# Optimization experiments

Hardware: AMD Instinct MI355X
Metric: run time of the kernel (lower is better)

## Reference

```python
import jax, jax.numpy as jnp
import numpy as np

B, T = 16, 100
MCL = 100      # MAX_CODE_LEN
D_IN = 200     # input_dim (= ques_encoding)
D_BERT = 768
KC = 50        # KC_one_hot_dim
KCD = 100      # kc_embed_dim
HID = 128
SCALE_BERT = 100
TW = 0.5       # QPALA_config.total_attention_weight
BTW = 0.5      # BLAA_config.total_attention_weight


def setup_inputs():
    key = jax.random.key(0)
    ks = jax.random.split(key, 20)
    f32 = jnp.float32
    # composite input feature vector: [ques_enc | code2vec idx | bert | time | score | kc one-hot]
    rnn_first = (jax.random.uniform(ks[0], (B, T, D_IN)) < 0.1).astype(f32)
    c2v = jax.random.randint(ks[1], (B, T, 3 * MCL), 0, 10000).astype(f32)
    bert = jax.random.normal(ks[2], (B, T, D_BERT), f32)
    time_f = jax.random.uniform(ks[3], (B, T, 10), f32)
    score_f = jax.random.uniform(ks[4], (B, T, 2), f32)
    kc = (jax.random.uniform(ks[5], (B, T, KC)) < 0.15).astype(f32)
    x = jnp.concatenate([rnn_first, c2v, bert, time_f, score_f, kc], axis=2)  # [B,T,1330]
    s = 0.05
    p = lambda k, shp: jax.random.normal(k, shp, f32) * s
    return dict(
        x=x,
        node_emb=p(ks[6], (10002, 100)),
        path_emb=p(ks[7], (20002, 100)),
        Wb=p(ks[8], (SCALE_BERT, D_BERT)), bb=jnp.zeros((SCALE_BERT,), f32),
        Wna=p(ks[9], (500, 500)), bna=jnp.zeros((500,), f32),
        Wia=p(ks[10], (KCD, 500)), bia=jnp.zeros((KCD,), f32),
        Wattn=p(ks[11], (1, 500)), battn=jnp.zeros((1,), f32),
        kc_emb=p(ks[12], (KC, KCD)),
        Wt=p(ks[13], (1, SCALE_BERT + KC + KCD)), bt=jnp.zeros((1,), f32),
        Wih=p(ks[14], (4 * HID, 950)), Whh=p(ks[15], (4 * HID, HID)),
        bih=jnp.zeros((4 * HID,), f32), bhh=jnp.zeros((4 * HID,), f32),
        Wfc=p(ks[16], (100, HID + KC + D_IN)), bfc=jnp.zeros((100,), f32),
    )


def _lstm(xseq, Wih, Whh, bih, bhh):
    # PyTorch LSTM, gate order i,f,g,o; batch_first
    bsz = xseq.shape[0]
    pre = jnp.einsum('btd,gd->btg', xseq, Wih) + bih + bhh  # [B,T,4H]

    def step(carry, g_in):
        h, c = carry
        g = g_in + h @ Whh.T
        i, f, gg, o = jnp.split(g, 4, axis=-1)
        c = jax.nn.sigmoid(f) * c + jax.nn.sigmoid(i) * jnp.tanh(gg)
        h = jax.nn.sigmoid(o) * jnp.tanh(c)
        return (h, c), h

    init = (jnp.zeros((bsz, HID), xseq.dtype), jnp.zeros((bsz, HID), xseq.dtype))
    _, hs = jax.lax.scan(step, init, jnp.swapaxes(pre, 0, 1))
    return jnp.swapaxes(hs, 0, 1)


def _forward(x, node_emb, path_emb, Wb, bb, Wna, bna, Wia, bia, Wattn, battn,
             kc_emb, Wt, bt, Wih, Whh, bih, bhh, Wfc, bfc):
    b, t = x.shape[0], x.shape[1]
    rnn_first = x[:, :, :D_IN]
    bert = x[:, :, 500:500 + D_BERT]
    kc_part = x[:, :, 1280:1280 + KC]
    c2v = x[:, :, D_IN:D_IN + 3 * MCL].reshape(b, t, MCL, 3).astype(jnp.int32)
    # gather embeddings + broadcast encoding -> full_embed [B,T,MCL,500]
    full = jnp.concatenate([
        node_emb[c2v[..., 0]], node_emb[c2v[..., 2]], path_emb[c2v[..., 1]],
        jnp.broadcast_to(rnn_first[:, :, None, :], (b, t, MCL, D_IN))], axis=3)
    bert_vec = bert @ Wb.T + bb  # [B,T,100]
    # non-interactive attention pooling (NB: original softmaxes over dim=1 = time)
    cw = jnp.tanh(full @ Wna.T + bna) @ Wattn.T + battn  # [B,T,MCL,1]
    aw = jax.nn.softmax(cw, axis=1)
    na = jnp.sum(full * aw, axis=2)  # [B,T,500]
    kcn = jnp.sum(kc_part, axis=2, keepdims=True)
    kcn = jnp.where(kcn == 0, 1.0, kcn)
    # interactive (KC) cross attention
    trans = full @ Wia.T + bia  # [B,T,MCL,KCD]
    Q = kc_part[..., None] * kc_emb[None, None]  # [B,T,KC,KCD]
    attn = jax.nn.softmax(jnp.einsum('btkd,btmd->btkm', Q, trans), axis=-1)
    Hm = jnp.einsum('btkm,btmd->btkd', attn, trans) * kc_part[..., None]
    ia = jnp.sum(Hm, axis=2) / kcn  # [B,T,KCD]
    rnn_input = jnp.concatenate([kc_part, rnn_first, ia, na, bert_vec], axis=2)  # [B,T,950]
    lstm_out = _lstm(rnn_input, Wih, Whh, bih, bhh)  # [B,T,HID]
    # per-time-step causal attention over lstm_out (vectorized form of the python loop)
    w = (jnp.concatenate([bert_vec, kc_part, ia], axis=2) @ Wt.T + bt)[..., 0]  # [B,T]
    mask = jnp.tril(jnp.ones((t, t), bool))
    logits = jnp.where(mask[None], w[:, None, :], -1e30)
    cattn = jax.nn.softmax(logits, axis=-1)  # [B,T,T]
    cur = jnp.einsum('bij,bjh->bih', cattn, lstm_out)
    attended = lstm_out * (1.0 - TW)
    attended = attended.at[:, 0].set(lstm_out[:, 0])
    idx = jnp.arange(t)
    addm = ((idx >= 1) & (idx <= t - 2)).astype(x.dtype)[None, :, None]
    attended = attended + cur * BTW * addm
    out = jax.nn.sigmoid(
        jnp.concatenate([rnn_first, kc_part, attended], axis=2) @ Wfc.T + bfc)
    return out  # [B,T,100]


def reference(x, node_emb, path_emb, Wb, bb, Wna, bna, Wia, bia, Wattn, battn,
              kc_emb, Wt, bt, Wih, Whh, bih, bhh, Wfc, bfc):
    return _forward(x, node_emb, path_emb, Wb, bb, Wna, bna, Wia, bia, Wattn, battn,
                    kc_emb, Wt, bt, Wih, Whh, bih, bhh, Wfc, bfc)
```

## Files before the change

### kernel.cpp

```cpp
#include <hip/hip_runtime.h>
#include <math.h>

typedef unsigned short ushort_t;
typedef unsigned char uchar_t;
typedef __attribute__((ext_vector_type(8))) short bf16x8;
typedef __attribute__((ext_vector_type(4))) float f32x4;

constexpr int CB = 16, CT = 100, CMCL = 100, CDIN = 200;
constexpr int CKC = 50, CHID = 128;
constexpr int XCH = 1330;
constexpr int NBT = CB * CT;
constexpr int NNODE = 10002, NPATH = 20002;
constexpr int TRS = 114;
constexpr int HSTR = 136;
constexpr int NT8_W = 1024;
constexpr int NTB_W = 512;
constexpr int PT8_W = 512;
constexpr int PTB_W = 256;
constexpr int XR_W  = 640;

__device__ __forceinline__ float frcp(float v){ return __builtin_amdgcn_rcpf(v); }
__device__ __forceinline__ float fsigmoid(float v){ return frcp(1.f + __expf(-v)); }
__device__ __forceinline__ float ftanh_(float v){
  float e = __expf(-2.f*fabsf(v));
  return copysignf((1.f - e) * frcp(1.f + e), v);
}
__device__ __forceinline__ float wredsum(float v){
  #pragma unroll
  for (int off = 32; off; off >>= 1) v += __shfl_xor(v, off);
  return v;
}
__device__ __forceinline__ float wredmax(float v){
  #pragma unroll
  for (int off = 32; off; off >>= 1) v = fmaxf(v, __shfl_xor(v, off));
  return v;
}
__device__ __forceinline__ ushort_t f2b(float f){
  union { float f; unsigned u; } c{f};
  return (ushort_t)((c.u + 0x7FFFu + ((c.u >> 16) & 1u)) >> 16);
}
__device__ __forceinline__ float b2f(unsigned hbits){
  union { unsigned u; float f; } c{hbits << 16};
  return c.f;
}
__device__ __forceinline__ void b8f(const ushort_t* p, float* o){
  uint4 v = *reinterpret_cast<const uint4*>(p);
  o[0]=b2f(v.x & 0xFFFFu); o[1]=b2f(v.x >> 16);
  o[2]=b2f(v.y & 0xFFFFu); o[3]=b2f(v.y >> 16);
  o[4]=b2f(v.z & 0xFFFFu); o[5]=b2f(v.z >> 16);
  o[6]=b2f(v.w & 0xFFFFu); o[7]=b2f(v.w >> 16);
}
__device__ __forceinline__ uchar_t ff8(float f){
  union { float f; unsigned u; } c{f};
  unsigned s = (c.u >> 24) & 0x80u;
  c.u &= 0x7FFFFFFFu;
  float a = c.f;
  unsigned b;
  if (a < 0.015625f) {
    b = (unsigned)(a * 512.f + 0.5f);
  } else {
    unsigned u = c.u + (0x0007FFFFu + ((c.u >> 20) & 1u));
    int e = (int)(u >> 23) - 120;
    unsigned mm = (u >> 20) & 7u;
    if (e >= 16) { e = 15; mm = 6; }
    b = ((unsigned)e << 3) | mm;
  }
  return (uchar_t)(s | b);
}
__device__ __forceinline__ float f8d(unsigned b){
  unsigned e = (b >> 3) & 15u, m = b & 7u;
  union { unsigned u; float f; } c{((e + 120u) << 23) | (m << 20)};
  float v = e ? c.f : (float)m * 0.001953125f;
  return (b & 0x80u) ? -v : v;
}
__device__ __forceinline__ void f8x8(uint2 p, float* o){
  #pragma unroll
  for (int j = 0; j < 4; ++j) o[j]     = f8d((p.x >> (8*j)) & 255u);
  #pragma unroll
  for (int j = 0; j < 4; ++j) o[4 + j] = f8d((p.y >> (8*j)) & 255u);
}

struct GDesc {
  const float* A; const float* B; float* Cf; void* Cb;
  int lda, kOff, kMax, K, M, Npad, rbp, cb, nsplit, ldc, omode, blocks;
};
struct MegaArgs { GDesc d[6]; int nd; };

__global__ __launch_bounds__(256) void mega_gemm(MegaArgs args)
{
  constexpr int KS = 136;
  __shared__ ushort_t As[128*KS];
  __shared__ ushort_t Bs[128*KS];
  int id = blockIdx.x;
  int di = 0;
  while (di < args.nd-1 && id >= args.d[di].blocks) { id -= args.d[di].blocks; ++di; }
  GDesc g = args.d[di];
  const int per = g.rbp * g.cb;
  const int sp = id / per, r = id % per;
  const int xcd = r & 7, s2 = r >> 3;
  const int y = xcd + 8*(s2 / g.cb), cbi = s2 % g.cb;
  const int bm = y*128, bn = cbi*128;
  if (bm >= g.M) return;
  const int tid = threadIdx.x, lane = tid & 63, w = tid >> 6;
  const int wm = w & 1, wn = w >> 1;
  const int lr = lane & 15, lkq = lane >> 4;
  const int kbase = g.kOff + sp * g.K;
  const int hK = g.K >> 1;

  for (int f = tid; f < 128*hK; f += 256) {
    int row = f / hK, j2 = (f % hK)*2;
    int gm = bm + row;
    float2 va = make_float2(0.f,0.f);
    if (gm < g.M && kbase + j2 + 2 <= g.kMax)
      va = *reinterpret_cast<const float2*>(g.A + (long)gm*g.lda + kbase + j2);
    *reinterpret_cast<unsigned*>(&As[row*KS + j2]) = (unsigned)f2b(va.x) | ((unsigned)f2b(va.y)<<16);
    float2 vb = *reinterpret_cast<const float2*>(g.B + ((long)sp*g.Npad + bn + row)*g.K + j2);
    *reinterpret_cast<unsigned*>(&Bs[row*KS + j2]) = (unsigned)f2b(vb.x) | ((unsigned)f2b(vb.y)<<16);
  }
  const int padw = (128 - g.K) >> 1;
  for (int f = tid; f < 128*padw; f += 256) {
    int row = f / padw, jd = f % padw;
    *reinterpret_cast<unsigned*>(&As[row*KS + g.K + jd*2]) = 0u;
    *reinterpret_cast<unsigned*>(&Bs[row*KS + g.K + jd*2]) = 0u;
  }
  __syncthreads();

  f32x4 acc[4][4];
  #pragma unroll
  for (int i = 0; i < 4; ++i)
    #pragma unroll
    for (int j = 0; j < 4; ++j) acc[i][j] = f32x4{0.f,0.f,0.f,0.f};
  #pragma unroll
  for (int ks = 0; ks < 4; ++ks) {
    const int ko = ks*32 + lkq*8;
    bf16x8 af[4], bf[4];
    #pragma unroll
    for (int i = 0; i < 4; ++i)
      af[i] = *reinterpret_cast<const bf16x8*>(&As[(wm*64 + i*16 + lr)*KS + ko]);
    #pragma unroll
    for (int j = 0; j < 4; ++j)
      bf[j] = *reinterpret_cast<const bf16x8*>(&Bs[(wn*64 + j*16 + lr)*KS + ko]);
    #pragma unroll
    for (int i = 0; i < 4; ++i)
      #pragma unroll
      for (int j = 0; j < 4; ++j)
        acc[i][j] = __builtin_amdgcn_mfma_f32_16x16x32_bf16(af[i], bf[j], acc[i][j], 0, 0, 0);
  }
  #pragma unroll
  for (int i = 0; i < 4; ++i) {
    #pragma unroll
    for (int j = 0; j < 4; ++j) {
      #pragma unroll
      for (int rr = 0; rr < 4; ++rr) {
        int gr = bm + wm*64 + i*16 + lkq*4 + rr;
        int gc = bn + wn*64 + j*16 + lr;
        if (gr < g.M) {
          float v = acc[i][j][rr];
          if (g.omode == 2)      ((uchar_t*)g.Cb)[(long)gr * g.ldc + gc] = ff8(v);
          else if (g.omode == 1) ((ushort_t*)g.Cb)[(long)gr * g.ldc + gc] = f2b(v);
          else                   g.Cf[((long)sp*g.M + gr)*g.ldc + gc] = v;
        }
      }
    }
  }
}

constexpr long PK_E0 = 1024L*100;
constexpr long PK_E1 = PK_E0 + 512L*100;
constexpr long PK_E2 = PK_E1 + 512L*100;
constexpr long PK_E3 = PK_E2 + 256L*100;
constexpr long PK_E4 = PK_E3 + 2L*XR_W*100;
constexpr long PK_E5 = PK_E4 + 6L*128*128;
constexpr long PK_E6 = PK_E5 + 10L*512*96;
constexpr long PK_E7 = PK_E6 + 512;
constexpr long PK_E8 = PK_E7 + 378L*100;

__global__ void pack_all(
    const float* __restrict__ Wna, const float* __restrict__ Wia,
    const float* __restrict__ bna, const float* __restrict__ bia,
    const float* __restrict__ Wb, const float* __restrict__ Wih,
    const float* __restrict__ Wattn, const float* __restrict__ Wfc,
    float* __restrict__ Bn8, float* __restrict__ Bnb,
    float* __restrict__ Bp8, float* __restrict__ Bpb,
    float* __restrict__ XB2, float* __restrict__ bias_x,
    float* __restrict__ BertB, float* __restrict__ P2B,
    ushort_t* __restrict__ WAB, float* __restrict__ WfcT)
{
  long i = (long)blockIdx.x*256 + threadIdx.x;
  if (i < PK_E0) {
    int n = (int)(i / 100), k = (int)(i % 100);
    float v = 0.f;
    if (n < 500)                    v = Wna[(long)n*500 + k];
    else if (n >= 512 && n < 1012)  v = Wna[(long)(n-512)*500 + 100 + k];
    Bn8[i] = v;
  } else if (i < PK_E1) {
    long j = i - PK_E0;
    int n = (int)(j / 100), k = (int)(j % 100);
    float v = 0.f;
    if (n < 100)                    v = (k == n) ? 1.f : 0.f;
    else if (n >= 112 && n < 212)   v = Wia[(long)(n-112)*500 + k];
    else if (n >= 256 && n < 356)   v = (k == n-256) ? 1.f : 0.f;
    else if (n >= 368 && n < 468)   v = Wia[(long)(n-368)*500 + 100 + k];
    Bnb[j] = v;
  } else if (i < PK_E2) {
    long j = i - PK_E1;
    int n = (int)(j / 100), k = (int)(j % 100);
    Bp8[j] = (n < 500) ? Wna[(long)n*500 + 200 + k] : 0.f;
  } else if (i < PK_E3) {
    long j = i - PK_E2;
    int n = (int)(j / 100), k = (int)(j % 100);
    float v = 0.f;
    if (n < 100)                    v = (k == n) ? 1.f : 0.f;
    else if (n >= 112 && n < 212)   v = Wia[(long)(n-112)*500 + 200 + k];
    Bpb[j] = v;
  } else if (i < PK_E4) {
    long j = i - PK_E3;
    if (j < XR_W) {
      float b = 0.f;
      if (j < 500) b = bna[j];
      else if (j >= 512 && j < 612) b = bia[j-512];
      bias_x[j] = b;
    }
    int s = (int)(j / (XR_W*100)), n = (int)((j / 100) % XR_W), k = (int)(j % 100);
    int k2 = s*100 + k;
    float v = 0.f;
    if (n < 500)                  v = Wna[(long)n*500 + 300 + k2];
    else if (n >= 512 && n < 612) v = Wia[(long)(n-512)*500 + 300 + k2];
    XB2[j] = v;
  } else if (i < PK_E5) {
    long j = i - PK_E4;
    int s = (int)(j / (128*128)), n = (int)((j / 128) % 128), k = (int)(j % 128);
    BertB[j] = (n < 100) ? Wb[(long)n*768 + s*128 + k] : 0.f;
  } else if (i < PK_E6) {
    long j = i - PK_E5;
    int s = (int)(j / (512*96)), n = (int)((j / 96) % 512), k = (int)(j % 96);
    int kg = s*96 + k;
    P2B[j] = (kg < 950) ? Wih[(long)n*950 + kg] : 0.f;
  } else if (i < PK_E7) {
    long j = i - PK_E6;
    WAB[j] = (j < 500) ? f2b(Wattn[j]) : (ushort_t)0;
  } else if (i < PK_E8) {
    long j = i - PK_E7;
    int o = (int)(j / 378), q = (int)(j % 378);
    WfcT[q*100 + o] = Wfc[j];
  }
}

__global__ __launch_bounds__(256) void reduce1(
    const float* __restrict__ xrP, const float* __restrict__ bias_x,
    uchar_t* __restrict__ XRF8, ushort_t* __restrict__ XRBF,
    const float* __restrict__ bertP, const float* __restrict__ bb, float* __restrict__ rnn)
{
  int bt = blockIdx.x, tid = threadIdx.x;
  for (int c = tid; c < XR_W; c += 256) {
    float v = xrP[(long)bt*XR_W + c] + xrP[((long)NBT + bt)*XR_W + c] + bias_x[c];
    if (c < 512) XRF8[(long)bt*512 + c] = ff8(v);
    else         XRBF[(long)bt*128 + (c - 512)] = f2b(v);
  }
  if (tid < 100) {
    float v = bb[tid];
    #pragma unroll
    for (int s = 0; s < 6; ++s) v += bertP[((long)s*NBT + bt)*128 + tid];
    rnn[(long)bt*950 + 850 + tid] = v;
  }
}

__global__ __launch_bounds__(512) void reduce_p2(
    const float* __restrict__ p2P, const float* __restrict__ bih, const float* __restrict__ bhh,
    ushort_t* __restrict__ P2)
{
  int bt = blockIdx.x, g = threadIdx.x;
  float v = bih[g] + bhh[g];
  #pragma unroll
  for (int s = 0; s < 10; ++s) v += p2P[((long)s*NBT + bt)*512 + g];
  int bq = bt / CT, tt = bt % CT;
  int q = g >> 7, rem = g & 127, ww = rem >> 4, lr2 = rem & 15;
  int lk2 = bq >> 2, rr = bq & 3;
  P2[((((long)tt*4 + q)*8 + ww)*4 + lk2)*64 + lr2*4 + rr] = f2b(v);
}

__global__ __launch_bounds__(256) void cw2_kernel(
    const float* __restrict__ x, const uchar_t* __restrict__ NT8,
    const uchar_t* __restrict__ PT8, const uchar_t* __restrict__ XRF8,
    const ushort_t* __restrict__ WAB,
    const float* __restrict__ battn, float* __restrict__ cwT)
{
  int bt = blockIdx.x, b = bt / CT, t = bt % CT;
  int tid = threadIdx.x, w = tid >> 6, lane = tid & 63;
  __shared__ int idx_s[300];
  for (int i = tid; i < 300; i += 256) idx_s[i] = (int)x[(long)bt*XCH + 200 + i];
  float rseg[8], wseg[8];
  f8x8(*reinterpret_cast<const uint2*>(XRF8 + (long)bt*512 + lane*8), rseg);
  b8f(WAB + lane*8, wseg);
  __syncthreads();
  float bat = battn[0];

  uint2 A0, C0, P0, A1, C1, P1;
  auto issue = [&](int m, uint2& A, uint2& C, uint2& P){
    if (m < CMCL) {
      int ai = idx_s[3*m], pi = idx_s[3*m+1], ci = idx_s[3*m+2];
      A = *reinterpret_cast<const uint2*>(NT8 + (long)ai*NT8_W + lane*8);
      C = *reinterpret_cast<const uint2*>(NT8 + (long)ci*NT8_W + 512 + lane*8);
      P = *reinterpret_cast<const uint2*>(PT8 + (long)pi*PT8_W + lane*8);
    }
  };
  auto proc = [&](int m, const uint2& A, const uint2& C, const uint2& P){
    if (m >= CMCL) return;
    float fa[8], fc[8], fp[8];
    f8x8(A, fa); f8x8(C, fc); f8x8(P, fp);
    float acc = 0.f;
    #pragma unroll
    for (int j = 0; j < 8; ++j)
      acc = fmaf(ftanh_(fa[j] + fc[j] + fp[j] + rseg[j]), wseg[j], acc);
    acc = wredsum(acc);
    if (lane == 0) cwT[((long)b*CMCL + m)*CT + t] = acc + bat;
  };

  issue(w, A0, C0, P0);
  for (int it = 0; it < 25; it += 2) {
    int m0 = w + it*4;
    issue(m0 + 4, A1, C1, P1);
    proc(m0, A0, C0, P0);
    issue(m0 + 8, A0, C0, P0);
    proc(m0 + 4, A1, C1, P1);
  }
}

__global__ void aw_kernel(const float* __restrict__ cwT, float* __restrict__ awT)
{
  int bm = blockIdx.x; int lane = threadIdx.x;
  const float* row = cwT + (long)bm * CT;
  bool h1 = lane < (CT - 64);
  float v0 = row[lane];
  float v1 = h1 ? row[64 + lane] : -3.0e38f;
  float mx = wredmax(fmaxf(v0, v1));
  float e0 = __expf(v0 - mx);
  float e1 = h1 ? __expf(v1 - mx) : 0.f;
  float s = wredsum(e0 + e1);
  float inv = frcp(s);
  awT[(long)bm*CT + lane] = e0 * inv;
  if (h1) awT[(long)bm*CT + 64 + lane] = e1 * inv;
}

__global__ __launch_bounds__(512) void fuse2_kernel(
    const float* __restrict__ x,
    const ushort_t* __restrict__ NTB, const ushort_t* __restrict__ PTB,
    const ushort_t* __restrict__ XRBF, const float* __restrict__ awT,
    const float* __restrict__ kc_emb, float* __restrict__ rnn,
    const float* __restrict__ Wt, const float* __restrict__ bt0, float* __restrict__ wbuf)
{
  int bt = blockIdx.x, b = bt / CT, t = bt % CT;
  int tid = threadIdx.x, w = tid >> 6, lane = tid & 63;
  int sub = lane >> 5, li = lane & 31;

  __shared__ ushort_t tr_s[100*TRS];
  __shared__ float nacc[8][344];
  __shared__ float ia_red[8][104];
  __shared__ float ia_f[100];
  __shared__ float aw_s[100];
  __shared__ int   idx_s[300];
  __shared__ float kcl[CKC];
  __shared__ int   act_k[CKC];
  __shared__ int   nact_s;
  __shared__ float kcn_s, awsum_s;

  for (int i = tid; i < 300; i += 512) idx_s[i] = (int)x[(long)bt*XCH + 200 + i];
  if (tid < 100) aw_s[tid] = awT[((long)b*CMCL + tid)*CT + t];
  if (tid < CKC) kcl[tid] = x[(long)bt*XCH + 1280 + tid];
  __syncthreads();
  if (tid == 0) {
    float kcn = 0.f; int na = 0;
    for (int k = 0; k < CKC; ++k) { float v = kcl[k]; kcn += v; if (v != 0.f) act_k[na++] = k; }
    nact_s = na; kcn_s = (kcn == 0.f) ? 1.f : kcn;
    float s = 0.f;
    for (int m = 0; m < CMCL; ++m) s += aw_s[m];
    awsum_s = s;
  }
  float rwseg[8];
  if (li >= 14 && li < 28) b8f(XRBF + (long)bt*128 + (li-14)*8, rwseg);
  __syncthreads();

  float na_a[8] = {}, na_c[8] = {}, na_p[8] = {};
  const bool gv = (li < 28);
  uint4 A0, C0, P0, A1, C1, P1;
  auto g_issue = [&](int m, uint4& A, uint4& C, uint4& P){
    if (m < CMCL && gv) {
      int ai = idx_s[3*m], pi = idx_s[3*m+1], ci = idx_s[3*m+2];
      A = *reinterpret_cast<const uint4*>(NTB + (long)ai*NTB_W + li*8);
      C = *reinterpret_cast<const uint4*>(NTB + (long)ci*NTB_W + 256 + li*8);
      P = *reinterpret_cast<const uint4*>(PTB + (long)pi*PTB_W + li*8);
    }
  };
  auto g_proc = [&](int m, const uint4& A, const uint4& C, const uint4& P){
    if (m >= CMCL || !gv) return;
    const unsigned ua[4] = {A.x, A.y, A.z, A.w};
    const unsigned uc[4] = {C.x, C.y, C.z, C.w};
    const unsigned up[4] = {P.x, P.y, P.z, P.w};
    if (li < 14) {
      float awm = aw_s[m];
      #pragma unroll
      for (int jj = 0; jj < 4; ++jj) {
        na_a[2*jj]   = fmaf(awm, b2f(ua[jj] & 0xffffu), na_a[2*jj]);
        na_a[2*jj+1] = fmaf(awm, b2f(ua[jj] >> 16),     na_a[2*jj+1]);
        na_c[2*jj]   = fmaf(awm, b2f(uc[jj] & 0xffffu), na_c[2*jj]);
        na_c[2*jj+1] = fmaf(awm, b2f(uc[jj] >> 16),     na_c[2*jj+1]);
        na_p[2*jj]   = fmaf(awm, b2f(up[jj] & 0xffffu), na_p[2*jj]);
        na_p[2*jj+1] = fmaf(awm, b2f(up[jj] >> 16),     na_p[2*jj+1]);
      }
    } else {
      unsigned* d32 = reinterpret_cast<unsigned*>(&tr_s[m*TRS + (li-14)*8]);
      #pragma unroll
      for (int jj = 0; jj < 4; ++jj) {
        float lo = b2f(ua[jj] & 0xffffu) + b2f(uc[jj] & 0xffffu) + b2f(up[jj] & 0xffffu) + rwseg[2*jj];
        float hi = b2f(ua[jj] >> 16)     + b2f(uc[jj] >> 16)     + b2f(up[jj] >> 16)     + rwseg[2*jj+1];
        d32[jj] = (unsigned)f2b(lo) | ((unsigned)f2b(hi) << 16);
      }
    }
  };
  const int mb = w*2 + sub;
  g_issue(mb, A0, C0, P0);
  for (int it = 0; it < 8; it += 2) {
    g_issue((it+1)*16 + mb, A1, C1, P1);
    g_proc(it*16 + mb, A0, C0, P0);
    g_issue((it+2)*16 + mb, A0, C0, P0);
    g_proc((it+1)*16 + mb, A1, C1, P1);
  }
  #pragma unroll
  for (int j = 0; j < 8; ++j) {
    na_a[j] += __shfl_xor(na_a[j], 32);
    na_c[j] += __shfl_xor(na_c[j], 32);
    na_p[j] += __shfl_xor(na_p[j], 32);
  }
  if (lane < 14) {
    #pragma unroll
    for (int j = 0; j < 8; ++j) {
      nacc[w][      lane*8 + j] = na_a[j];
      nacc[w][112 + lane*8 + j] = na_c[j];
      nacc[w][224 + lane*8 + j] = na_p[j];
    }
  }
  __syncthreads();

  for (int q = tid; q < 336; q += 512) {
    float v = 0.f;
    #pragma unroll
    for (int ww2 = 0; ww2 < 8; ++ww2) v += nacc[ww2][q];
    int seg = q / 112, col = q % 112;
    if (col < 100) rnn[(long)bt*950 + 350 + seg*100 + col] = v;
  }
  for (int q = tid; q < CDIN; q += 512) {
    float xv = x[(long)bt*XCH + q];
    rnn[(long)bt*950 + 50 + q] = xv;
    rnn[(long)bt*950 + 650 + q] = awsum_s * xv;
  }
  if (tid < CKC) rnn[(long)bt*950 + tid] = kcl[tid];

  float ia0 = 0.f, ia1 = 0.f;
  const bool vrow1 = lane < 36;
  const bool vpv   = lane < 50;
  const int nact = nact_s;
  const unsigned* tr32_0 = reinterpret_cast<const unsigned*>(&tr_s[lane*TRS]);
  const unsigned* tr32_1 = reinterpret_cast<const unsigned*>(&tr_s[(64+lane)*TRS]);
  const unsigned* tr32   = reinterpret_cast<const unsigned*>(tr_s);
  for (int ki = w; ki < nact; ki += 8) {
    int k = act_k[ki];
    float kck = kcl[k];
    const float* ke = kc_emb + (long)k*100;
    float s0 = 0.f, s1 = 0.f;
    #pragma unroll 5
    for (int dh = 0; dh < 50; ++dh) {
      float k0 = ke[2*dh], k1 = ke[2*dh+1];
      unsigned u0 = tr32_0[dh];
      s0 = fmaf(k0, b2f(u0 & 0xffffu), s0);
      s0 = fmaf(k1, b2f(u0 >> 16), s0);
      if (vrow1) {
        unsigned u1 = tr32_1[dh];
        s1 = fmaf(k0, b2f(u1 & 0xffffu), s1);
        s1 = fmaf(k1, b2f(u1 >> 16), s1);
      }
    }
    s0 *= kck; s1 *= kck;
    float mx = wredmax(fmaxf(s0, vrow1 ? s1 : -3.0e38f));
    float p0e = __expf(s0 - mx);
    float p1e = vrow1 ? __expf(s1 - mx) : 0.f;
    float sm = wredsum(p0e + p1e);
    float inv = kck * frcp(sm);
    p0e *= inv; p1e *= inv;
    #pragma unroll 4
    for (int m = 0; m < CMCL; ++m) {
      float pm = (m < 64) ? __shfl(p0e, m) : __shfl(p1e, m - 64);
      if (vpv) {
        unsigned u = tr32[m*57 + lane];
        ia0 = fmaf(pm, b2f(u & 0xffffu), ia0);
        ia1 = fmaf(pm, b2f(u >> 16), ia1);
      }
    }
  }
  if (vpv) { ia_red[w][2*lane] = ia0; ia_red[w][2*lane+1] = ia1; }
  __syncthreads();
  if (tid < 100) {
    float v = 0.f;
    #pragma unroll
    for (int ww2 = 0; ww2 < 8; ++ww2) v += ia_red[ww2][tid];
    v *= frcp(kcn_s);
    rnn[(long)bt*950 + 250 + tid] = v;
    ia_f[tid] = v;
  }
  __syncthreads();
  if (tid < 64) {
    float acc = 0.f;
    for (int i = tid; i < 250; i += 64) {
      float f;
      if (i < 100)      f = rnn[(long)bt*950 + 850 + i];
      else if (i < 150) f = kcl[i - 100];
      else              f = ia_f[i - 150];
      acc = fmaf(Wt[i], f, acc);
    }
    acc = wredsum(acc);
    if (tid == 0) wbuf[bt] = acc + bt0[0];
  }
}

__global__ __launch_bounds__(512) void lstm_mfma2(
    const ushort_t* __restrict__ P2,
    const float* __restrict__ Whh,
    float* __restrict__ lstm_out)
{
  const int tid = threadIdx.x, lane = tid & 63, w = tid >> 6;
  const int lr = lane & 15, lkq = lane >> 4;
  __shared__ ushort_t H[2][16 * HSTR];
  {
    ushort_t* hp = &H[0][0];
    for (int i = tid; i < 2*16*HSTR; i += 512) hp[i] = 0;
  }

  bf16x8 bw0[4], bw1[4], bw2[4], bw3[4];
  #pragma unroll
  for (int kk = 0; kk < 4; ++kk) {
    short s[8];
    const float* wp0 = Whh + (long)(0*128 + w*16 + lr) * 128 + kk*32 + lkq*8;
    const float* wp1 = Whh + (long)(1*128 + w*16 + lr) * 128 + kk*32 + lkq*8;
    const float* wp2 = Whh + (long)(2*128 + w*16 + lr) * 128 + kk*32 + lkq*8;
    const float* wp3 = Whh + (long)(3*128 + w*16 + lr) * 128 + kk*32 + lkq*8;
    #pragma unroll
    for (int j = 0; j < 8; ++j) s[j] = (short)f2b(wp0[j]);
    bw0[kk] = bf16x8{s[0],s[1],s[2],s[3],s[4],s[5],s[6],s[7]};
    #pragma unroll
    for (int j = 0; j < 8; ++j) s[j] = (short)f2b(wp1[j]);
    bw1[kk] = bf16x8{s[0],s[1],s[2],s[3],s[4],s[5],s[6],s[7]};
    #pragma unroll
    for (int j = 0; j < 8; ++j) s[j] = (short)f2b(wp2[j]);
    bw2[kk] = bf16x8{s[0],s[1],s[2],s[3],s[4],s[5],s[6],s[7]};
    #pragma unroll
    for (int j = 0; j < 8; ++j) s[j] = (short)f2b(wp3[j]);
    bw3[kk] = bf16x8{s[0],s[1],s[2],s[3],s[4],s[5],s[6],s[7]};
  }

  auto pptr = [&](int t, int q){
    return reinterpret_cast<const uint2*>(P2 + (((((long)t*4 + q)*8 + w)*4 + lkq)*64 + lr*4));
  };
  uint2 pc0 = *pptr(0,0), pc1 = *pptr(0,1), pc2 = *pptr(0,2), pc3 = *pptr(0,3);
  uint2 pn0, pn1, pn2, pn3;
  f32x4 c = {0.f,0.f,0.f,0.f};
  __syncthreads();

  int pb = 0;
  for (int t = 0; t < CT; ++t) {
    if (t + 1 < CT) { pn0 = *pptr(t+1,0); pn1 = *pptr(t+1,1); pn2 = *pptr(t+1,2); pn3 = *pptr(t+1,3); }
    bf16x8 a[4];
    #pragma unroll
    for (int kk = 0; kk < 4; ++kk)
      a[kk] = *reinterpret_cast<const bf16x8*>(&H[pb][lr*HSTR + kk*32 + lkq*8]);
    f32x4 acc0 = f32x4{ b2f(pc0.x & 0xffffu), b2f(pc0.x >> 16), b2f(pc0.y & 0xffffu), b2f(pc0.y >> 16) };
    f32x4 acc1 = f32x4{ b2f(pc1.x & 0xffffu), b2f(pc1.x >> 16), b2f(pc1.y & 0xffffu), b2f(pc1.y >> 16) };
    f32x4 acc2 = f32x4{ b2f(pc2.x & 0xffffu), b2f(pc2.x >> 16), b2f(pc2.y & 0xffffu), b2f(pc2.y >> 16) };
    f32x4 acc3 = f32x4{ b2f(pc3.x & 0xffffu), b2f(pc3.x >> 16), b2f(pc3.y & 0xffffu), b2f(pc3.y >> 16) };
    #pragma unroll
    for (int kk = 0; kk < 4; ++kk) {
      acc0 = __builtin_amdgcn_mfma_f32_16x16x32_bf16(a[kk], bw0[kk], acc0, 0,0,0);
      acc1 = __builtin_amdgcn_mfma_f32_16x16x32_bf16(a[kk], bw1[kk], acc1, 0,0,0);
      acc2 = __builtin_amdgcn_mfma_f32_16x16x32_bf16(a[kk], bw2[kk], acc2, 0,0,0);
      acc3 = __builtin_amdgcn_mfma_f32_16x16x32_bf16(a[kk], bw3[kk], acc3, 0,0,0);
    }
    #pragma unroll
    for (int r = 0; r < 4; ++r) {
      float ig = fsigmoid(acc0[r]);
      float fg = fsigmoid(acc1[r]);
      float gg = ftanh_(acc2[r]);
      float og = fsigmoid(acc3[r]);
      c[r] = fg*c[r] + ig*gg;
      float h = og * ftanh_(c[r]);
      int row = lkq*4 + r;
      H[pb^1][row*HSTR + w*16 + lr] = f2b(h);
      lstm_out[((long)row*CT + t)*128 + w*16 + lr] = h;
    }
    __syncthreads();
    pb ^= 1;
    pc0 = pn0; pc1 = pn1; pc2 = pn2; pc3 = pn3;
  }
}

__global__ __launch_bounds__(256) void final_kernel(
    const float* __restrict__ x, const float* __restrict__ wbuf,
    const float* __restrict__ lstm_out, const float* __restrict__ WfcT,
    const float* __restrict__ bfc, float* __restrict__ out)
{
  int bt = blockIdx.x; int b = bt / CT, i = bt % CT;
  int tid = threadIdx.x;
  __shared__ float p_s[CT];
  __shared__ float feat_s[384];
  if (tid < 64) {
    bool h1 = (64 + tid) < CT;
    float v0 = (tid <= i) ? wbuf[(long)b*CT + tid] : -3.0e38f;
    float v1 = (h1 && (64 + tid) <= i) ? wbuf[(long)b*CT + 64 + tid] : -3.0e38f;
    float mx = wredmax(fmaxf(v0, v1));
    float e0 = (tid <= i) ? __expf(v0 - mx) : 0.f;
    float e1 = (h1 && (64 + tid) <= i) ? __expf(v1 - mx) : 0.f;
    float s = wredsum(e0 + e1);
    float inv = frcp(s);
    p_s[tid] = e0 * inv;
    if (h1) p_s[64 + tid] = e1 * inv;
  }
  __syncthreads();
  if (tid < CHID) {
    float cur = 0.f;
    #pragma unroll 4
    for (int j = 0; j <= i; ++j) cur = fmaf(p_s[j], lstm_out[((long)b*CT + j)*CHID + tid], cur);
    float l = lstm_out[((long)b*CT + i)*CHID + tid];
    float att;
    if (i == 0) att = l;
    else { att = 0.5f * l; if (i <= CT - 2) att = fmaf(0.5f, cur, att); }
    feat_s[250 + tid] = att;
  }
  for (int q = tid; q < 250; q += 256)
    feat_s[q] = (q < 200) ? x[(long)bt*XCH + q] : x[(long)bt*XCH + 1280 + (q - 200)];
  __syncthreads();
  if (tid < 100) {
    float acc = bfc[tid];
    #pragma unroll 4
    for (int q = 0; q < 378; ++q) acc = fmaf(WfcT[q*100 + tid], feat_s[q], acc);
    out[(long)bt*100 + tid] = fsigmoid(acc);
  }
}

extern "C" void kernel_launch(void* const* d_in, const int* in_sizes, int n_in,
                              void* d_out, int out_size, void* d_ws, size_t ws_size,
                              hipStream_t stream) {
  (void)in_sizes; (void)n_in; (void)out_size; (void)ws_size;
  const float* x        = (const float*)d_in[0];
  const float* node_emb = (const float*)d_in[1];
  const float* path_emb = (const float*)d_in[2];
  const float* Wb       = (const float*)d_in[3];
  const float* bb       = (const float*)d_in[4];
  const float* Wna      = (const float*)d_in[5];
  const float* bna      = (const float*)d_in[6];
  const float* Wia      = (const float*)d_in[7];
  const float* bia      = (const float*)d_in[8];
  const float* Wattn    = (const float*)d_in[9];
  const float* battn    = (const float*)d_in[10];
  const float* kc_emb   = (const float*)d_in[11];
  const float* Wt       = (const float*)d_in[12];
  const float* bt0      = (const float*)d_in[13];
  const float* Wih      = (const float*)d_in[14];
  const float* Whh      = (const float*)d_in[15];
  const float* bih      = (const float*)d_in[16];
  const float* bhh      = (const float*)d_in[17];
  const float* Wfc      = (const float*)d_in[18];
  const float* bfc      = (const float*)d_in[19];
  float* out = (float*)d_out;

  char* cur = (char*)d_ws;
  auto alloc = [&](size_t bytes)->char* {
    char* p = cur; cur += (bytes + 255) & ~(size_t)255; return p;
  };
  uchar_t* NT8   = (uchar_t*)alloc((size_t)NNODE*NT8_W);
  ushort_t* NTB  = (ushort_t*)alloc((size_t)NNODE*NTB_W*2);
  uchar_t* PT8   = (uchar_t*)alloc((size_t)NPATH*PT8_W);
  ushort_t* PTB  = (ushort_t*)alloc((size_t)NPATH*PTB_W*2);
  uchar_t* XRF8  = (uchar_t*)alloc((size_t)NBT*512);
  ushort_t* XRBF = (ushort_t*)alloc((size_t)NBT*128*2);
  float* Bn8    = (float*)alloc((size_t)1024*100*4);
  float* Bnb    = (float*)alloc((size_t)512*100*4);
  float* Bp8    = (float*)alloc((size_t)512*100*4);
  float* Bpb    = (float*)alloc((size_t)256*100*4);
  float* XB2    = (float*)alloc((size_t)2*XR_W*100*4);
  float* BertB  = (float*)alloc((size_t)6*128*128*4);
  float* P2B    = (float*)alloc((size_t)10*512*96*4);
  float* bias_x = (float*)alloc((size_t)XR_W*4);
  ushort_t* WAB = (ushort_t*)alloc(512*2);
  float* cwT  = (float*)alloc((size_t)NBT*100*4);
  float* awT  = (float*)alloc((size_t)NBT*100*4);
  float* rnn  = (float*)alloc((size_t)NBT*950*4);
  char*  uni  = alloc((size_t)10*NBT*512*4);
  float* xrP   = (float*)uni;
  float* bertP = (float*)(uni + (size_t)2*NBT*XR_W*4);
  float* p2P   = (float*)uni;
  ushort_t* P2 = (ushort_t*)alloc((size_t)NBT*512*2);
  float* lstm = (float*)alloc((size_t)NBT*128*4);
  float* wbuf = (float*)alloc((size_t)NBT*4);
  float* WfcT = (float*)alloc((size_t)378*100*4);

  pack_all<<<(unsigned)((PK_E8 + 255)/256), 256, 0, stream>>>(
      Wna, Wia, bna, bia, Wb, Wih, Wattn, Wfc,
      Bn8, Bnb, Bp8, Bpb, XB2, bias_x, BertB, P2B, WAB, WfcT);

  {
    MegaArgs a{};
    a.nd = 6;
    a.d[0] = { node_emb, Bn8, nullptr, NT8,  100, 0, 100, 100, NNODE, 1024, 80, 8, 1, 1024, 2, 80*8 };
    a.d[1] = { node_emb, Bnb, nullptr, NTB,  100, 0, 100, 100, NNODE, 512,  80, 4, 1, 512,  1, 80*4 };
    a.d[2] = { path_emb, Bp8, nullptr, PT8,  100, 0, 100, 100, NPATH, 512, 160, 4, 1, 512,  2, 160*4 };
    a.d[3] = { path_emb, Bpb, nullptr, PTB,  100, 0, 100, 100, NPATH, 256, 160, 2, 1, 256,  1, 160*2 };
    a.d[4] = { x, BertB, bertP, nullptr, XCH, 500, 1268, 128, NBT, 128, 16, 1, 6, 128, 0, 16*1*6 };
    a.d[5] = { x, XB2,   xrP,   nullptr, XCH, 0,   200,  100, NBT, XR_W, 16, 5, 2, XR_W, 0, 16*5*2 };
    int total = 0;
    for (int i2 = 0; i2 < 6; ++i2) total += a.d[i2].blocks;
    mega_gemm<<<total, 256, 0, stream>>>(a);
  }
  reduce1<<<NBT, 256, 0, stream>>>(xrP, bias_x, XRF8, XRBF, bertP, bb, rnn);

  cw2_kernel<<<NBT,256,0,stream>>>(x, NT8, PT8, XRF8, WAB, battn, cwT);
  aw_kernel<<<CB*CMCL,64,0,stream>>>(cwT, awT);
  fuse2_kernel<<<NBT,512,0,stream>>>(x, NTB, PTB, XRBF, awT, kc_emb, rnn, Wt, bt0, wbuf);

  {
    MegaArgs a{};
    a.nd = 1;
    a.d[0] = { rnn, P2B, p2P, nullptr, 950, 0, 950, 96, NBT, 512, 16, 4, 10, 512, 0, 16*4*10 };
    mega_gemm<<<a.d[0].blocks, 256, 0, stream>>>(a);
  }
  reduce_p2<<<NBT, 512, 0, stream>>>(p2P, bih, bhh, P2);

  lstm_mfma2<<<1,512,0,stream>>>(P2, Whh, lstm);
  final_kernel<<<NBT,256,0,stream>>>(x, wbuf, lstm, WfcT, bfc, out);
}
```

Before: 562.6 us.

## Simplify fp8 codec, shrink node bf16 table, store XR as bf16, halve fuse2 block

Replaces the branchy fp8 encode/decode with branch-free bit arithmetic that unpacks two bytes at a time. Drops the redundant identity block from the node bf16 table, shrinking it from 512 to 384 columns to cut GEMM work and gather bandwidth. Stores the XR activations as a single bf16 buffer instead of mixed fp8/bf16, which gives the cw2 row segment more precision but more bytes. Runs fuse2 with 256 threads instead of 512, lowering parallelism per block while changing reduction widths.

```diff
diff --git a/kernel.cpp b/kernel.cpp
--- a/kernel.cpp
+++ b/kernel.cpp
@@ -14,7 +14,7 @@
 constexpr int TRS = 114;
 constexpr int HSTR = 136;
 constexpr int NT8_W = 1024;
-constexpr int NTB_W = 512;
+constexpr int NTB_W = 384;
 constexpr int PT8_W = 512;
 constexpr int PTB_W = 256;
 constexpr int XR_W  = 640;
@@ -53,31 +53,23 @@
 __device__ __forceinline__ uchar_t ff8(float f){
   union { float f; unsigned u; } c{f};
   unsigned s = (c.u >> 24) & 0x80u;
-  c.u &= 0x7FFFFFFFu;
-  float a = c.f;
-  unsigned b;
-  if (a < 0.015625f) {
-    b = (unsigned)(a * 512.f + 0.5f);
-  } else {
-    unsigned u = c.u + (0x0007FFFFu + ((c.u >> 20) & 1u));
-    int e = (int)(u >> 23) - 120;
-    unsigned mm = (u >> 20) & 7u;
-    if (e >= 16) { e = 15; mm = 6; }
-    b = ((unsigned)e << 3) | mm;
-  }
-  return (uchar_t)(s | b);
-}
-__device__ __forceinline__ float f8d(unsigned b){
-  unsigned e = (b >> 3) & 15u, m = b & 7u;
-  union { unsigned u; float f; } c{((e + 120u) << 23) | (m << 20)};
-  float v = e ? c.f : (float)m * 0.001953125f;
-  return (b & 0x80u) ? -v : v;
-}
-__device__ __forceinline__ void f8x8(uint2 p, float* o){
-  #pragma unroll
-  for (int j = 0; j < 4; ++j) o[j]     = f8d((p.x >> (8*j)) & 255u);
-  #pragma unroll
-  for (int j = 0; j < 4; ++j) o[4 + j] = f8d((p.y >> (8*j)) & 255u);
+  unsigned a = c.u & 0x7FFFFFFFu;
+  a = a < 0x3C000000u ? 0x3C000000u : a;
+  a = a + 0x0007FFFFu + ((a >> 20) & 1u);
+  a = a > 0x43E00000u ? 0x43E00000u : a;
+  return (uchar_t)(s | (((a >> 20) - 0x3C0u) & 0x7Fu));
+}
+__device__ __forceinline__ void f8x8f(uint2 p, float* o){
+  #pragma unroll
+  for (int h = 0; h < 2; ++h) {
+    unsigned w = h ? p.y : p.x;
+    unsigned d0 = (w & 0xFFu) | ((w & 0xFF00u) << 8);
+    unsigned d1 = ((w >> 16) & 0xFFu) | ((w >> 8) & 0x00FF0000u);
+    unsigned v0 = ((d0 & 0x00800080u) << 8) | (((d0 & 0x007F007Fu) << 4) + 0x3C003C00u);
+    unsigned v1 = ((d1 & 0x00800080u) << 8) | (((d1 & 0x007F007Fu) << 4) + 0x3C003C00u);
+    union { unsigned u; float f; } c0{v0 << 16}, c1{v0 & 0xFFFF0000u}, c2{v1 << 16}, c3{v1 & 0xFFFF0000u};
+    o[4*h+0] = c0.f; o[4*h+1] = c1.f; o[4*h+2] = c2.f; o[4*h+3] = c3.f;
+  }
 }
 
 struct GDesc {
@@ -166,7 +158,7 @@
 }
 
 constexpr long PK_E0 = 1024L*100;
-constexpr long PK_E1 = PK_E0 + 512L*100;
+constexpr long PK_E1 = PK_E0 + 384L*100;
 constexpr long PK_E2 = PK_E1 + 512L*100;
 constexpr long PK_E3 = PK_E2 + 256L*100;
 constexpr long PK_E4 = PK_E3 + 2L*XR_W*100;
@@ -199,8 +191,7 @@
     float v = 0.f;
     if (n < 100)                    v = (k == n) ? 1.f : 0.f;
     else if (n >= 112 && n < 212)   v = Wia[(long)(n-112)*500 + k];
-    else if (n >= 256 && n < 356)   v = (k == n-256) ? 1.f : 0.f;
-    else if (n >= 368 && n < 468)   v = Wia[(long)(n-368)*500 + 100 + k];
+    else if (n >= 224 && n < 324)   v = Wia[(long)(n-224)*500 + 100 + k];
     Bnb[j] = v;
   } else if (i < PK_E2) {
     long j = i - PK_E1;
@@ -247,15 +238,13 @@
 }
 
 __global__ __launch_bounds__(256) void reduce1(
-    const float* __restrict__ xrP, const float* __restrict__ bias_x,
-    uchar_t* __restrict__ XRF8, ushort_t* __restrict__ XRBF,
+    const float* __restrict__ xrP, const float* __restrict__ bias_x, ushort_t* __restrict__ XR,
     const float* __restrict__ bertP, const float* __restrict__ bb, float* __restrict__ rnn)
 {
   int bt = blockIdx.x, tid = threadIdx.x;
   for (int c = tid; c < XR_W; c += 256) {
     float v = xrP[(long)bt*XR_W + c] + xrP[((long)NBT + bt)*XR_W + c] + bias_x[c];
-    if (c < 512) XRF8[(long)bt*512 + c] = ff8(v);
-    else         XRBF[(long)bt*128 + (c - 512)] = f2b(v);
+    XR[(long)bt*XR_W + c] = f2b(v);
   }
   if (tid < 100) {
     float v = bb[tid];
@@ -281,7 +270,7 @@
 
 __global__ __launch_bounds__(256) void cw2_kernel(
     const float* __restrict__ x, const uchar_t* __restrict__ NT8,
-    const uchar_t* __restrict__ PT8, const uchar_t* __restrict__ XRF8,
+    const uchar_t* __restrict__ PT8, const ushort_t* __restrict__ XR,
     const ushort_t* __restrict__ WAB,
     const float* __restrict__ battn, float* __restrict__ cwT)
 {
@@ -290,7 +279,7 @@
   __shared__ int idx_s[300];
   for (int i = tid; i < 300; i += 256) idx_s[i] = (int)x[(long)bt*XCH + 200 + i];
   float rseg[8], wseg[8];
-  f8x8(*reinterpret_cast<const uint2*>(XRF8 + (long)bt*512 + lane*8), rseg);
+  b8f(XR + (long)bt*XR_W + lane*8, rseg);
   b8f(WAB + lane*8, wseg);
   __syncthreads();
   float bat = battn[0];
@@ -307,7 +296,7 @@
   auto proc = [&](int m, const uint2& A, const uint2& C, const uint2& P){
     if (m >= CMCL) return;
     float fa[8], fc[8], fp[8];
-    f8x8(A, fa); f8x8(C, fc); f8x8(P, fp);
+    f8x8f(A, fa); f8x8f(C, fc); f8x8f(P, fp);
     float acc = 0.f;
     #pragma unroll
     for (int j = 0; j < 8; ++j)
@@ -342,10 +331,10 @@
   if (h1) awT[(long)bm*CT + 64 + lane] = e1 * inv;
 }
 
-__global__ __launch_bounds__(512) void fuse2_kernel(
+__global__ __launch_bounds__(256) void fuse2_kernel(
     const float* __restrict__ x,
     const ushort_t* __restrict__ NTB, const ushort_t* __restrict__ PTB,
-    const ushort_t* __restrict__ XRBF, const float* __restrict__ awT,
+    const ushort_t* __restrict__ XR, const float* __restrict__ awT,
     const float* __restrict__ kc_emb, float* __restrict__ rnn,
     const float* __restrict__ Wt, const float* __restrict__ bt0, float* __restrict__ wbuf)
 {
@@ -354,8 +343,8 @@
   int sub = lane >> 5, li = lane & 31;
 
   __shared__ ushort_t tr_s[100*TRS];
-  __shared__ float nacc[8][344];
-  __shared__ float ia_red[8][104];
+  __shared__ float nacc[4][344];
+  __shared__ float ia_red[4][104];
   __shared__ float ia_f[100];
   __shared__ float aw_s[100];
   __shared__ int   idx_s[300];
@@ -364,7 +353,7 @@
   __shared__ int   nact_s;
   __shared__ float kcn_s, awsum_s;
 
-  for (int i = tid; i < 300; i += 512) idx_s[i] = (int)x[(long)bt*XCH + 200 + i];
+  for (int i = tid; i < 300; i += 256) idx_s[i] = (int)x[(long)bt*XCH + 200 + i];
   if (tid < 100) aw_s[tid] = awT[((long)b*CMCL + tid)*CT + t];
   if (tid < CKC) kcl[tid] = x[(long)bt*XCH + 1280 + tid];
   __syncthreads();
@@ -377,7 +366,7 @@
     awsum_s = s;
   }
   float rwseg[8];
-  if (li >= 14 && li < 28) b8f(XRBF + (long)bt*128 + (li-14)*8, rwseg);
+  if (li >= 14 && li < 28) b8f(XR + (long)bt*XR_W + 512 + (li-14)*8, rwseg);
   __syncthreads();
 
   float na_a[8] = {}, na_c[8] = {}, na_p[8] = {};
@@ -386,9 +375,11 @@
   auto g_issue = [&](int m, uint4& A, uint4& C, uint4& P){
     if (m < CMCL && gv) {
       int ai = idx_s[3*m], pi = idx_s[3*m+1], ci = idx_s[3*m+2];
-      A = *reinterpret_cast<const uint4*>(NTB + (long)ai*NTB_W + li*8);
-      C = *reinterpret_cast<const uint4*>(NTB + (long)ci*NTB_W + 256 + li*8);
-      P = *reinterpret_cast<const uint4*>(PTB + (long)pi*PTB_W + li*8);
+      int offA = li*8;
+      int offC = li*8 + ((li < 14) ? 0 : 112);
+      A = *reinterpret_cast<const uint4*>(NTB + (long)ai*NTB_W + offA);
+      C = *reinterpret_cast<const uint4*>(NTB + (long)ci*NTB_W + offC);
+      P = *reinterpret_cast<const uint4*>(PTB + (long)pi*PTB_W + offA);
     }
   };
   auto g_proc = [&](int m, const uint4& A, const uint4& C, const uint4& P){
@@ -419,11 +410,11 @@
   };
   const int mb = w*2 + sub;
   g_issue(mb, A0, C0, P0);
-  for (int it = 0; it < 8; it += 2) {
-    g_issue((it+1)*16 + mb, A1, C1, P1);
-    g_proc(it*16 + mb, A0, C0, P0);
-    g_issue((it+2)*16 + mb, A0, C0, P0);
-    g_proc((it+1)*16 + mb, A1, C1, P1);
+  for (int it = 0; it < 13; it += 2) {
+    g_issue((it+1)*8 + mb, A1, C1, P1);
+    g_proc(it*8 + mb, A0, C0, P0);
+    g_issue((it+2)*8 + mb, A0, C0, P0);
+    g_proc((it+1)*8 + mb, A1, C1, P1);
   }
   #pragma unroll
   for (int j = 0; j < 8; ++j) {
@@ -441,14 +432,12 @@
   }
   __syncthreads();
 
-  for (int q = tid; q < 336; q += 512) {
-    float v = 0.f;
-    #pragma unroll
-    for (int ww2 = 0; ww2 < 8; ++ww2) v += nacc[ww2][q];
+  for (int q = tid; q < 336; q += 256) {
+    float v = nacc[0][q] + nacc[1][q] + nacc[2][q] + nacc[3][q];
     int seg = q / 112, col = q % 112;
     if (col < 100) rnn[(long)bt*950 + 350 + seg*100 + col] = v;
   }
-  for (int q = tid; q < CDIN; q += 512) {
+  for (int q = tid; q < CDIN; q += 256) {
     float xv = x[(long)bt*XCH + q];
     rnn[(long)bt*950 + 50 + q] = xv;
     rnn[(long)bt*950 + 650 + q] = awsum_s * xv;
@@ -462,7 +451,7 @@
   const unsigned* tr32_0 = reinterpret_cast<const unsigned*>(&tr_s[lane*TRS]);
   const unsigned* tr32_1 = reinterpret_cast<const unsigned*>(&tr_s[(64+lane)*TRS]);
   const unsigned* tr32   = reinterpret_cast<const unsigned*>(tr_s);
-  for (int ki = w; ki < nact; ki += 8) {
+  for (int ki = w; ki < nact; ki += 4) {
     int k = act_k[ki];
     float kck = kcl[k];
     const float* ke = kc_emb + (long)k*100;
@@ -499,10 +488,7 @@
   if (vpv) { ia_red[w][2*lane] = ia0; ia_red[w][2*lane+1] = ia1; }
   __syncthreads();
   if (tid < 100) {
-    float v = 0.f;
-    #pragma unroll
-    for (int ww2 = 0; ww2 < 8; ++ww2) v += ia_red[ww2][tid];
-    v *= frcp(kcn_s);
+    float v = (ia_red[0][tid] + ia_red[1][tid] + ia_red[2][tid] + ia_red[3][tid]) * frcp(kcn_s);
     rnn[(long)bt*950 + 250 + tid] = v;
     ia_f[tid] = v;
   }
@@ -677,10 +663,9 @@
   ushort_t* NTB  = (ushort_t*)alloc((size_t)NNODE*NTB_W*2);
   uchar_t* PT8   = (uchar_t*)alloc((size_t)NPATH*PT8_W);
   ushort_t* PTB  = (ushort_t*)alloc((size_t)NPATH*PTB_W*2);
-  uchar_t* XRF8  = (uchar_t*)alloc((size_t)NBT*512);
-  ushort_t* XRBF = (ushort_t*)alloc((size_t)NBT*128*2);
+  ushort_t* XR   = (ushort_t*)alloc((size_t)NBT*XR_W*2);
   float* Bn8    = (float*)alloc((size_t)1024*100*4);
-  float* Bnb    = (float*)alloc((size_t)512*100*4);
+  float* Bnb    = (float*)alloc((size_t)384*100*4);
   float* Bp8    = (float*)alloc((size_t)512*100*4);
   float* Bpb    = (float*)alloc((size_t)256*100*4);
   float* XB2    = (float*)alloc((size_t)2*XR_W*100*4);
@@ -708,7 +693,7 @@
     MegaArgs a{};
     a.nd = 6;
     a.d[0] = { node_emb, Bn8, nullptr, NT8,  100, 0, 100, 100, NNODE, 1024, 80, 8, 1, 1024, 2, 80*8 };
-    a.d[1] = { node_emb, Bnb, nullptr, NTB,  100, 0, 100, 100, NNODE, 512,  80, 4, 1, 512,  1, 80*4 };
+    a.d[1] = { node_emb, Bnb, nullptr, NTB,  100, 0, 100, 100, NNODE, 384,  80, 3, 1, 384,  1, 80*3 };
     a.d[2] = { path_emb, Bp8, nullptr, PT8,  100, 0, 100, 100, NPATH, 512, 160, 4, 1, 512,  2, 160*4 };
     a.d[3] = { path_emb, Bpb, nullptr, PTB,  100, 0, 100, 100, NPATH, 256, 160, 2, 1, 256,  1, 160*2 };
     a.d[4] = { x, BertB, bertP, nullptr, XCH, 500, 1268, 128, NBT, 128, 16, 1, 6, 128, 0, 16*1*6 };
@@ -717,11 +702,11 @@
     for (int i2 = 0; i2 < 6; ++i2) total += a.d[i2].blocks;
     mega_gemm<<<total, 256, 0, stream>>>(a);
   }
-  reduce1<<<NBT, 256, 0, stream>>>(xrP, bias_x, XRF8, XRBF, bertP, bb, rnn);
-
-  cw2_kernel<<<NBT,256,0,stream>>>(x, NT8, PT8, XRF8, WAB, battn, cwT);
+  reduce1<<<NBT, 256, 0, stream>>>(xrP, bias_x, XR, bertP, bb, rnn);
+
+  cw2_kernel<<<NBT,256,0,stream>>>(x, NT8, PT8, XR, WAB, battn, cwT);
   aw_kernel<<<CB*CMCL,64,0,stream>>>(cwT, awT);
-  fuse2_kernel<<<NBT,512,0,stream>>>(x, NTB, PTB, XRBF, awT, kc_emb, rnn, Wt, bt0, wbuf);
+  fuse2_kernel<<<NBT,256,0,stream>>>(x, NTB, PTB, XR, awT, kc_emb, rnn, Wt, bt0, wbuf);
 
   {
     MegaArgs a{};
```

Measured after the change: 516.1 us. 1.09x faster.
